# Kernel optimization log

Hardware: AMD Instinct MI355X
Metric: run time of the kernel (lower is better)

The kernel has to match this reference:

```python
import jax, jax.numpy as jnp
import numpy as np

B, T, D = 2, 2048, 2048
H = 16
DK = 64          # head_k_dim (key_dim = D*0.5 = 1024)
DV = 128         # head_v_dim (value_dim = D*1.0 = 2048)
R = 16           # gate_low_rank_dim
GLN = 16.0       # gate_logit_normalizer
C = 64           # chunk size
EPS = 1e-5


def setup_inputs() -> dict:
    key = jax.random.key(0)
    ks = jax.random.split(key, 12)
    s = 0.02
    return {
        "hidden_states": jax.random.normal(ks[0], (B, T, D), jnp.float32),
        "Wq": jax.random.normal(ks[1], (D, H * DK), jnp.float32) * s,
        "Wk": jax.random.normal(ks[2], (D, H * DK), jnp.float32) * s,
        "Wv": jax.random.normal(ks[3], (D, H * DV), jnp.float32) * s,
        "Wgk1": jax.random.normal(ks[4], (D, R), jnp.float32) * s,
        "Wgk2": jax.random.normal(ks[5], (R, H * DK), jnp.float32) * s,
        "bgk2": jnp.zeros((H * DK,), jnp.float32),
        "Wg1": jax.random.normal(ks[6], (D, R), jnp.float32) * s,
        "Wg2": jax.random.normal(ks[7], (R, H * DV), jnp.float32) * s,
        "bg2": jnp.zeros((H * DV,), jnp.float32),
        "Wo": jax.random.normal(ks[8], (H * DV, D), jnp.float32) * s,
        "gnorm_w": jnp.ones((DV,), jnp.float32),
    }


def _gla_chunk(q, k, v, gk):
    """Chunked gated linear attention.
    q,k,gk: [B,T,H,DK], v: [B,T,H,DV]. Recurrence:
    S_t = diag(exp(gk_t)) S_{t-1} + k_t v_t^T ; o_t = q_t @ S_t.
    """
    nC = T // C
    # [nC, B, H, C, d]
    def to_chunks(x):
        return x.reshape(B, nC, C, H, -1).transpose(1, 0, 3, 2, 4)
    qc, kc, vc, gkc = map(to_chunks, (q, k, v, gk))
    Gc = jnp.cumsum(gkc, axis=3)  # inclusive cumsum of log-decays within chunk
    tri = jnp.tril(jnp.ones((C, C), bool))

    def step(S, inp):
        q_c, k_c, v_c, G_c = inp  # [B,H,C,dk] / [B,H,C,dv]
        qg = q_c * jnp.exp(G_c)            # decays <= 0 within chunk -> safe
        kg = k_c * jnp.exp(-G_c)
        # inter-chunk: state contribution
        o = jnp.einsum('bhcd,bhde->bhce', qg, S)
        # intra-chunk causal attention with decay
        A = jnp.einsum('bhid,bhjd->bhij', qg, kg)
        A = jnp.where(tri, A, 0.0)
        o = o + jnp.einsum('bhij,bhje->bhie', A, v_c)
        # state update
        G_last = G_c[:, :, -1, :]                       # [B,H,dk]
        k_dec = k_c * jnp.exp(G_last[:, :, None, :] - G_c)
        S = S * jnp.exp(G_last)[:, :, :, None] + jnp.einsum('bhcd,bhce->bhde', k_dec, v_c)
        return S, o

    S0 = jnp.zeros((B, H, DK, DV), q.dtype)
    _, o = jax.lax.scan(step, S0, (qc, kc, vc, Gc))
    # [nC,B,H,C,dv] -> [B,T,H,dv]
    return o.transpose(1, 0, 3, 2, 4).reshape(B, T, H, DV)


def reference(hidden_states, Wq, Wk, Wv, Wgk1, Wgk2, bgk2, Wg1, Wg2, bg2, Wo, gnorm_w):
    hs = hidden_states
    q = jax.nn.silu(hs @ Wq).reshape(B, T, H, DK)
    k = jax.nn.silu(hs @ Wk).reshape(B, T, H, DK)
    v = jax.nn.silu(hs @ Wv).reshape(B, T, H, DV)
    gk = ((hs @ Wgk1) @ Wgk2 + bgk2).reshape(B, T, H, DK)
    gk = jax.nn.log_sigmoid(gk) / GLN
    q = q * (DK ** -0.5)  # fla default scale
    o = _gla_chunk(q, k, v, gk)  # [B,T,H,DV]
    # RMSNorm over head_v_dim
    o = o * jax.lax.rsqrt(jnp.mean(o * o, axis=-1, keepdims=True) + EPS) * gnorm_w
    g = ((hs @ Wg1) @ Wg2 + bg2).reshape(B, T, H, DV)
    o = o * jax.nn.sigmoid(g)
    return o.reshape(B, T, H * DV) @ Wo
```

## Files before the change

### kernel.cpp

```cpp
#include <hip/hip_runtime.h>
#include <cstdint>

#define Bq   2
#define Tq   2048
#define Dq   2048
#define Hq   16
#define DKq  64
#define DVq  128
#define Cq   64
#define NCq  32
#define Mq   4096
#define NBH  32

typedef _Float16 f16;
typedef f16 f16x4 __attribute__((ext_vector_type(4)));
typedef f16 f16x8 __attribute__((ext_vector_type(8)));
typedef float f32x4 __attribute__((ext_vector_type(4)));
typedef unsigned short u16;
typedef u16 u16x8 __attribute__((ext_vector_type(8)));

__device__ __forceinline__ void gl_lds16(const void* g, void* l) {
    __builtin_amdgcn_global_load_lds(
        (const __attribute__((address_space(1))) uint32_t*)g,
        (__attribute__((address_space(3))) uint32_t*)l, 16, 0, 0);
}

#define BARX()   asm volatile("s_barrier" ::: "memory")
#define LGKM0()  asm volatile("s_waitcnt lgkmcnt(0)" ::: "memory")
#define VMW8()   asm volatile("s_waitcnt vmcnt(8)" ::: "memory")
#define VMW6()   asm volatile("s_waitcnt vmcnt(6)" ::: "memory")

__global__ __launch_bounds__(256) void trans_all(const float* __restrict__ Wq,
                                                 const float* __restrict__ Wk,
                                                 const float* __restrict__ Wv,
                                                 const float* __restrict__ Wo,
                                                 f16* __restrict__ Qkv, f16* __restrict__ WoT) {
    __shared__ float sh[4096];
    int blk = blockIdx.x;
    int tid = threadIdx.x;
    const float* W; f16* Dh; int N, nt, kt; long rowoff;
    if (blk < 2048)      { W = Wq; N = 1024; int t = blk;        nt = t & 31; kt = t >> 5; Dh = Qkv; rowoff = 0; }
    else if (blk < 4096) { W = Wk; N = 1024; int t = blk - 2048; nt = t & 31; kt = t >> 5; Dh = Qkv; rowoff = 1024; }
    else if (blk < 8192) { W = Wv; N = 2048; int t = blk - 4096; nt = t & 63; kt = t >> 6; Dh = Qkv; rowoff = 2048; }
    else                 { W = Wo; N = 2048; int t = blk - 8192; nt = t & 63; kt = t >> 6; Dh = WoT; rowoff = 0; }
    int tx = tid & 31, ty = tid >> 5;
#pragma unroll
    for (int i = 0; i < 4; i++) {
        int k = kt * 32 + ty + i * 8;
        int n = nt * 32 + tx;
        sh[tx * 33 + ty + i * 8] = W[(long)k * N + n];
    }
    __syncthreads();
#pragma unroll
    for (int i = 0; i < 4; i++) {
        int n = nt * 32 + ty + i * 8;
        int k = kt * 32 + tx;
        Dh[(rowoff + n) * 2048L + k] = (f16)sh[(ty + i * 8) * 33 + tx];
    }
}

__global__ __launch_bounds__(256) void hs_conv(const float* __restrict__ in,
                                               f16* __restrict__ out) {
    long i = ((long)blockIdx.x * 256 + threadIdx.x) * 8;
    float4 a = *(const float4*)(in + i);
    float4 b = *(const float4*)(in + i + 4);
    f16x8 h;
    h[0] = (f16)a.x; h[1] = (f16)a.y; h[2] = (f16)a.z; h[3] = (f16)a.w;
    h[4] = (f16)b.x; h[5] = (f16)b.y; h[6] = (f16)b.z; h[7] = (f16)b.w;
    *(f16x8*)(out + i) = h;
}

__global__ __launch_bounds__(256) void lowrank_tg(const float* __restrict__ hs,
                                                  const float* __restrict__ Wgk1,
                                                  const float* __restrict__ Wg1,
                                                  float* __restrict__ t_gk,
                                                  float* __restrict__ t_g) {
    __shared__ float sW[512 * 32];
    int tid = threadIdx.x;
    int blk = blockIdx.x;
    int r = tid >> 4, seg = tid & 15;
    long row = (long)blk * 16 + r;
    float acc[32];
#pragma unroll
    for (int c = 0; c < 32; c++) acc[c] = 0.f;
    for (int kc = 0; kc < 2048; kc += 512) {
        __syncthreads();
#pragma unroll
        for (int i = 0; i < 16; i++) {
            int s = tid + i * 256;
            int k = s >> 3, q = s & 7;
            float4 w = (q < 4) ? *(const float4*)(Wgk1 + (long)(kc + k) * 16 + q * 4)
                               : *(const float4*)(Wg1  + (long)(kc + k) * 16 + (q - 4) * 4);
            int qs = q ^ ((k >> 5) & 7);
            *(float4*)&sW[k * 32 + qs * 4] = w;
        }
        __syncthreads();
        const float* hp = hs + row * 2048 + kc + seg * 32;
        int xr = seg & 7;
#pragma unroll
        for (int k4 = 0; k4 < 8; k4++) {
            float4 hv = *(const float4*)(hp + k4 * 4);
            float hvv[4] = {hv.x, hv.y, hv.z, hv.w};
#pragma unroll
            for (int u = 0; u < 4; u++) {
                int k = seg * 32 + k4 * 4 + u;
                const float* wr = &sW[k * 32];
#pragma unroll
                for (int q = 0; q < 8; q++) {
                    float4 wv = *(const float4*)(wr + ((q ^ xr) * 4));
                    acc[q * 4 + 0] += hvv[u] * wv.x;
                    acc[q * 4 + 1] += hvv[u] * wv.y;
                    acc[q * 4 + 2] += hvv[u] * wv.z;
                    acc[q * 4 + 3] += hvv[u] * wv.w;
                }
            }
        }
    }
#pragma unroll
    for (int c = 0; c < 32; c++) {
        acc[c] += __shfl_xor(acc[c], 1);
        acc[c] += __shfl_xor(acc[c], 2);
        acc[c] += __shfl_xor(acc[c], 4);
        acc[c] += __shfl_xor(acc[c], 8);
    }
    if (seg == 0) {
        float4 a;
        a.x = acc[0];  a.y = acc[1];  a.z = acc[2];  a.w = acc[3];  *(float4*)(t_gk + row * 16)     = a;
        a.x = acc[4];  a.y = acc[5];  a.z = acc[6];  a.w = acc[7];  *(float4*)(t_gk + row * 16 + 4) = a;
        a.x = acc[8];  a.y = acc[9];  a.z = acc[10]; a.w = acc[11]; *(float4*)(t_gk + row * 16 + 8) = a;
        a.x = acc[12]; a.y = acc[13]; a.z = acc[14]; a.w = acc[15]; *(float4*)(t_gk + row * 16 + 12)= a;
        a.x = acc[16]; a.y = acc[17]; a.z = acc[18]; a.w = acc[19]; *(float4*)(t_g + row * 16)      = a;
        a.x = acc[20]; a.y = acc[21]; a.z = acc[22]; a.w = acc[23]; *(float4*)(t_g + row * 16 + 4)  = a;
        a.x = acc[24]; a.y = acc[25]; a.z = acc[26]; a.w = acc[27]; *(float4*)(t_g + row * 16 + 8)  = a;
        a.x = acc[28]; a.y = acc[29]; a.z = acc[30]; a.w = acc[31]; *(float4*)(t_g + row * 16 + 12) = a;
    }
}

__global__ __launch_bounds__(512, 2) void gemm256q(const f16* __restrict__ A,
                                                   const f16* __restrict__ Bt,
                                                   f16* __restrict__ h0,
                                                   f16* __restrict__ h1,
                                                   f16* __restrict__ h2) {
    __shared__ __align__(16) f16 sA[2][16384];
    __shared__ __align__(16) f16 sB[2][16384];
    int tid = threadIdx.x;
    int wave = tid >> 6, lane = tid & 63;
    int quad = lane >> 4, l16 = lane & 15;
    int wm = wave >> 2, wn = wave & 3;

    int cpx = (int)gridDim.x >> 3;
    int wid = ((int)blockIdx.x & 7) * cpx + ((int)blockIdx.x >> 3);
    int bm = wid & 15, bn = wid >> 4;

    const f16* Ab = A  + (long)bm * 256 * 2048;
    const f16* Bb = Bt + (long)bn * 256 * 2048;

    int srow = tid >> 3;
    int gsrc = ((tid & 7) ^ (srow & 7)) * 8;
    const f16* Asrc = Ab + (long)srow * 2048 + gsrc;
    const f16* Bsrc = Bb + (long)srow * 2048 + gsrc;

#define STAGE(P, KT) do { \
    const f16* as_ = Asrc + (KT) * 64; \
    const f16* bs_ = Bsrc + (KT) * 64; \
    f16* la_ = &sA[P][tid * 8]; \
    f16* lb_ = &sB[P][tid * 8]; \
    _Pragma("unroll") \
    for (int q_ = 0; q_ < 4; q_++) gl_lds16(as_ + (long)q_ * 64 * 2048, la_ + q_ * 4096); \
    _Pragma("unroll") \
    for (int q_ = 0; q_ < 4; q_++) gl_lds16(bs_ + (long)q_ * 64 * 2048, lb_ + q_ * 4096); \
} while (0)

    int go0 = (quad ^ (l16 & 7)) * 8;
    int go1 = go0 ^ 32;
    const f16* aB0 = &sA[0][(wm * 128 + l16) * 64];
    const f16* aB1 = &sA[1][(wm * 128 + l16) * 64];
    const f16* bB0 = &sB[0][(wn * 64 + l16) * 64];
    const f16* bB1 = &sB[1][(wn * 64 + l16) * 64];

    f16x8 afr[4][2], bfr[2][2][2];
    f32x4 acc[8][4] = {};

#define LDA(PB, MH) do { \
    _Pragma("unroll") \
    for (int ii_ = 0; ii_ < 4; ii_++) { \
        afr[ii_][0] = *(const f16x8*)(PB + ((MH) * 4 + ii_) * 1024 + go0); \
        afr[ii_][1] = *(const f16x8*)(PB + ((MH) * 4 + ii_) * 1024 + go1); \
    } \
} while (0)

#define LDB(PB, NH) do { \
    _Pragma("unroll") \
    for (int jj_ = 0; jj_ < 2; jj_++) { \
        bfr[NH][jj_][0] = *(const f16x8*)(PB + ((NH) * 2 + jj_) * 1024 + go0); \
        bfr[NH][jj_][1] = *(const f16x8*)(PB + ((NH) * 2 + jj_) * 1024 + go1); \
    } \
} while (0)

#define QMFMA(MH, NH) do { \
    __builtin_amdgcn_s_setprio(1); \
    _Pragma("unroll") \
    for (int ii_ = 0; ii_ < 4; ii_++) \
    _Pragma("unroll") \
    for (int jj_ = 0; jj_ < 2; jj_++) { \
        acc[(MH)*4+ii_][(NH)*2+jj_] = __builtin_amdgcn_mfma_f32_16x16x32_f16(afr[ii_][0], bfr[NH][jj_][0], acc[(MH)*4+ii_][(NH)*2+jj_], 0, 0, 0); \
        acc[(MH)*4+ii_][(NH)*2+jj_] = __builtin_amdgcn_mfma_f32_16x16x32_f16(afr[ii_][1], bfr[NH][jj_][1], acc[(MH)*4+ii_][(NH)*2+jj_], 0, 0, 0); \
    } \
    __builtin_amdgcn_s_setprio(0); \
} while (0)

    STAGE(0, 0);
    STAGE(1, 1);
    VMW8();
    BARX();

#pragma unroll 1
    for (int it = 0; it < 16; it++) {
        int kt2 = 2 * it + 2; if (kt2 > 31) kt2 = 31;
        int kt3 = 2 * it + 3; if (kt3 > 31) kt3 = 31;
        LDA(aB0, 0); LDB(bB0, 0);
        BARX(); LGKM0(); QMFMA(0, 0); BARX();
        LDB(bB0, 1);
        BARX(); LGKM0(); QMFMA(0, 1); BARX();
        LDA(aB0, 1);
        BARX(); LGKM0(); QMFMA(1, 0); BARX();
        STAGE(0, kt2);
        VMW8();
        BARX(); QMFMA(1, 1); BARX();
        LDA(aB1, 0); LDB(bB1, 0);
        BARX(); LGKM0(); QMFMA(0, 0); BARX();
        LDB(bB1, 1);
        BARX(); LGKM0(); QMFMA(0, 1); BARX();
        LDA(aB1, 1);
        BARX(); LGKM0(); QMFMA(1, 0); BARX();
        STAGE(1, kt3);
        VMW8();
        BARX(); QMFMA(1, 1); BARX();
    }
    asm volatile("s_waitcnt vmcnt(0)" ::: "memory");

    long rb = (long)bm * 256 + wm * 128 + quad * 4;
    f16* dst; long cw, cb; float sc = 1.f;
    if (bn < 4)      { dst = h0; cw = 1024; cb = (long)bn * 256;       sc = 0.125f; }
    else if (bn < 8) { dst = h1; cw = 1024; cb = (long)(bn - 4) * 256; }
    else             { dst = h2; cw = 2048; cb = (long)(bn - 8) * 256; }
    long cbase = cb + wn * 64 + l16;
#pragma unroll
    for (int i = 0; i < 8; i++)
#pragma unroll
        for (int j = 0; j < 4; j++)
#pragma unroll
            for (int r = 0; r < 4; r++) {
                float x = acc[i][j][r];
                x = x / (1.f + __expf(-x)) * sc;
                dst[(rb + i * 16 + r) * cw + cbase + j * 16] = (f16)x;
            }
#undef STAGE
#undef LDA
#undef LDB
#undef QMFMA
}

__global__ __launch_bounds__(512, 2) void gemm128o(const f16* __restrict__ A,
                                                   const f16* __restrict__ Bt,
                                                   float* __restrict__ o0) {
    __shared__ __align__(16) f16 sAb[16384];
    __shared__ __align__(16) f16 sBb[32768];
    int tid = threadIdx.x;
    int wave = tid >> 6, lane = tid & 63;
    int quad = lane >> 4, l16 = lane & 15;
    int wm = wave >> 2, wn = wave & 3;

    int cpx = (int)gridDim.x >> 3;
    int wid = ((int)blockIdx.x & 7) * cpx + ((int)blockIdx.x >> 3);
    int bm = wid & 31, bn = wid >> 5;

    int srow = tid >> 3;
    int gsrc = ((tid & 7) ^ (srow & 7)) * 8;
    const f16* Asrc = A  + ((long)bm * 128 + srow) * 2048 + gsrc;
    const f16* Bsrc = Bt + ((long)bn * 256 + srow) * 2048 + gsrc;

#define STAGE(P, KT) do { \
    _Pragma("unroll") \
    for (int q_ = 0; q_ < 2; q_++) \
        gl_lds16(Asrc + (KT) * 64 + (long)q_ * 64 * 2048, sAb + (P) * 8192 + tid * 8 + q_ * 4096); \
    _Pragma("unroll") \
    for (int q_ = 0; q_ < 4; q_++) \
        gl_lds16(Bsrc + (KT) * 64 + (long)q_ * 64 * 2048, sBb + (P) * 16384 + tid * 8 + q_ * 4096); \
} while (0)

    int go0 = (quad ^ (l16 & 7)) * 8;
    int go1 = go0 ^ 32;
    const f16* pA0 = sAb + (wm * 64 + l16) * 64 + go0;
    const f16* pA1 = sAb + (wm * 64 + l16) * 64 + go1;
    const f16* pB0 = sBb + (wn * 64 + l16) * 64 + go0;
    const f16* pB1 = sBb + (wn * 64 + l16) * 64 + go1;

    f16x8 aX[4], bX[4], aY[4], bY[4];
    f32x4 acc[4][4] = {};

#define RDA(D, PTR, POFF) do { \
    D[0] = *(const f16x8*)((PTR) + (POFF)); \
    D[1] = *(const f16x8*)((PTR) + (POFF) + 1024); \
    D[2] = *(const f16x8*)((PTR) + (POFF) + 2048); \
    D[3] = *(const f16x8*)((PTR) + (POFF) + 3072); \
} while (0)

#define MM(AS, BS) do { \
    __builtin_amdgcn_s_setprio(1); \
    _Pragma("unroll") \
    for (int m_ = 0; m_ < 4; m_++) \
    _Pragma("unroll") \
    for (int n_ = 0; n_ < 4; n_++) \
        acc[m_][n_] = __builtin_amdgcn_mfma_f32_16x16x32_f16(AS[m_], BS[n_], acc[m_][n_], 0, 0, 0); \
    __builtin_amdgcn_s_setprio(0); \
} while (0)

    STAGE(0, 0);
    STAGE(1, 1);
    VMW6();
    BARX();
    RDA(aX, pA0, 0); RDA(bX, pB0, 0);

#pragma unroll 1
    for (int it = 0; it < 16; it++) {
        int c2 = 2 * it + 2; if (c2 > 31) c2 = 31;
        int c3 = 2 * it + 3; if (c3 > 31) c3 = 31;
        RDA(aY, pA1, 0); RDA(bY, pB1, 0);
        MM(aX, bX);
        LGKM0();
        BARX();
        STAGE(0, c2);
        VMW6();
        BARX();
        RDA(aX, pA0, 8192); RDA(bX, pB0, 16384);
        MM(aY, bY);
        RDA(aY, pA1, 8192); RDA(bY, pB1, 16384);
        MM(aX, bX);
        LGKM0();
        BARX();
        STAGE(1, c3);
        VMW6();
        BARX();
        RDA(aX, pA0, 0); RDA(bX, pB0, 0);
        MM(aY, bY);
    }
    asm volatile("s_waitcnt vmcnt(0)" ::: "memory");

    long rb = (long)bm * 128 + wm * 64 + quad * 4;
    long cbase = (long)bn * 256 + wn * 64 + l16;
#pragma unroll
    for (int m = 0; m < 4; m++)
#pragma unroll
        for (int n = 0; n < 4; n++)
#pragma unroll
            for (int r = 0; r < 4; r++)
                o0[(rb + m * 16 + r) * 2048 + cbase + n * 16] = acc[m][n][r];
#undef STAGE
#undef RDA
#undef MM
}

__global__ __launch_bounds__(256) void vtrans(const u16* __restrict__ v,
                                              u16* __restrict__ vT) {
    __shared__ uint32_t su[128 * 65];
    int tid = threadIdx.x;
    int t0 = (blockIdx.x >> 5) * 128;
    int e0 = (blockIdx.x & 31) * 64;
#pragma unroll
    for (int i = 0; i < 4; i++) {
        int tr = i * 32 + (tid >> 3);
        int ec = (tid & 7) * 8;
        u16x8 g = *(const u16x8*)(v + (long)(t0 + tr) * 2048 + e0 + ec);
#pragma unroll
        for (int j = 0; j < 8; j++) su[tr * 65 + ec + j] = g[j];
    }
    __syncthreads();
#pragma unroll
    for (int i = 0; i < 2; i++) {
        int er = i * 32 + (tid >> 3);
        int tch = (tid & 7) * 16;
        u16x8 o0, o1;
#pragma unroll
        for (int j = 0; j < 8; j++) {
            o0[j] = (u16)su[(tch + j) * 65 + er];
            o1[j] = (u16)su[(tch + 8 + j) * 65 + er];
        }
        u16* dst = vT + (long)(e0 + er) * 4096 + t0 + tch;
        *(u16x8*)dst = o0;
        *(u16x8*)(dst + 8) = o1;
    }
}

__global__ __launch_bounds__(256) void gk_cum(const float* __restrict__ t_gk,
                                              const float* __restrict__ Wgk2,
                                              const float* __restrict__ bgk2,
                                              float* __restrict__ G,
                                              float* __restrict__ dec) {
    __shared__ float sT[1024];
    __shared__ float sW[1024];
    __shared__ float sb[64];
    __shared__ float sG[64 * 64];
    int blk = blockIdx.x;
    int c = blk & 31, h = (blk >> 5) & 15, b = blk >> 9;
    int tid = threadIdx.x;
    long rowbase = (long)b * Tq + c * 64;
    {
        int idx = tid * 4;
        *(float4*)&sT[idx] = *(const float4*)(t_gk + rowbase * 16 + idx);
        int rr = idx >> 6, dd = idx & 63;
        *(float4*)&sW[idx] = *(const float4*)(Wgk2 + rr * 1024 + h * 64 + dd);
    }
    if (tid < 64) sb[tid] = bgk2[h * 64 + tid];
    __syncthreads();
    int tquad = tid >> 4, dgrp = tid & 15;
    float4 bg4 = *(float4*)&sb[dgrp * 4];
#pragma unroll
    for (int j = 0; j < 4; j++) {
        int t = tquad * 4 + j;
        float4 z = bg4;
#pragma unroll
        for (int rr = 0; rr < 16; rr++) {
            float tv = sT[t * 16 + rr];
            float4 wv = *(float4*)&sW[rr * 64 + dgrp * 4];
            z.x += tv * wv.x; z.y += tv * wv.y; z.z += tv * wv.z; z.w += tv * wv.w;
        }
        float4 o;
        o.x = (fminf(z.x, 0.f) - log1pf(__expf(-fabsf(z.x)))) * 0.0625f;
        o.y = (fminf(z.y, 0.f) - log1pf(__expf(-fabsf(z.y)))) * 0.0625f;
        o.z = (fminf(z.z, 0.f) - log1pf(__expf(-fabsf(z.z)))) * 0.0625f;
        o.w = (fminf(z.w, 0.f) - log1pf(__expf(-fabsf(z.w)))) * 0.0625f;
        *(float4*)&sG[t * 64 + dgrp * 4] = o;
    }
    __syncthreads();
    if (tid < 64) {
        float run = 0.f;
        for (int t = 0; t < 64; t++) { run += sG[t * 64 + tid]; sG[t * 64 + tid] = run; }
        dec[blk * 64 + tid] = __expf(run);
    }
    __syncthreads();
    float* Gb = G + (long)blk * 4096;
#pragma unroll
    for (int i = 0; i < 4; i++) {
        int f = tid + i * 256;
        *(float4*)(Gb + f * 4) = *(float4*)&sG[f * 4];
    }
}

#define ST 68
__global__ __launch_bounds__(256) void gla_pass1(const f16* __restrict__ kbuf,
                                                 const f16* __restrict__ vh,
                                                 const float* __restrict__ G,
                                                 float* __restrict__ U) {
    __shared__ float sG[64 * ST];
    __shared__ float sK[64 * ST];
    int blk = blockIdx.x;
    int c = blk & 31, h = (blk >> 5) & 15, b = blk >> 9;
    int tid = threadIdx.x;
    long rowbase = (long)b * Tq + c * 64;
    const float* Gb = G + (long)blk * 4096;
#pragma unroll
    for (int i = 0; i < 4; i++) {
        int f = tid + i * 256;
        float4 v = *(const float4*)(Gb + f * 4);
        int t = f >> 4, d0 = (f & 15) * 4;
        *(float4*)&sG[t * ST + d0] = v;
    }
    __syncthreads();
#pragma unroll
    for (int i = 0; i < 16; i++) {
        int idx = tid + i * 256;
        int t = idx >> 6, d = idx & 63;
        float gl = sG[63 * ST + d];
        sK[t * ST + d] = (float)kbuf[(rowbase + t) * 1024 + h * 64 + d] * __expf(gl - sG[t * ST + d]);
    }
    __syncthreads();
    int ty = tid >> 4, tx = tid & 15;
    float acc[4][8] = {};
    const f16* vb = vh + rowbase * 2048 + h * 128 + tx * 8;
    for (int t = 0; t < 64; t++) {
        float kd[4];
        *(float4*)&kd[0] = *(float4*)&sK[t * ST + ty * 4];
        f16x8 vv = *(const f16x8*)(vb + (long)t * 2048);
        float ve[8];
#pragma unroll
        for (int e = 0; e < 8; e++) ve[e] = (float)vv[e];
#pragma unroll
        for (int r = 0; r < 4; r++)
#pragma unroll
            for (int e = 0; e < 8; e++) acc[r][e] += kd[r] * ve[e];
    }
    float* Ub = U + (long)blk * 8192;
#pragma unroll
    for (int r = 0; r < 4; r++) {
        int d = ty * 4 + r;
#pragma unroll
        for (int e8 = 0; e8 < 8; e8++)
            Ub[(tx * 8 + e8) * 64 + d] = acc[r][e8];
    }
}

__global__ __launch_bounds__(256) void gla_pass2(const float* __restrict__ U,
                                                 const float* __restrict__ dec,
                                                 f16* __restrict__ ShT) {
    int bh = blockIdx.x >> 2;
    int tid = threadIdx.x;
    int e = (blockIdx.x & 3) * 32 + (tid >> 3);
    int d0 = (tid & 7) * 8;
    float4 Sa = {0.f, 0.f, 0.f, 0.f}, Sb = {0.f, 0.f, 0.f, 0.f};
    for (int c = 0; c < NCq; c++) {
        long base = ((long)(bh * 32 + c) * 128 + e) * 64 + d0;
        float4 u0 = *(const float4*)(U + base);
        float4 u1 = *(const float4*)(U + base + 4);
        const float* dp = dec + (bh * 32 + c) * 64 + d0;
        float4 dc0 = *(const float4*)dp;
        float4 dc1 = *(const float4*)(dp + 4);
        f16x8 sh;
        sh[0] = (f16)Sa.x; sh[1] = (f16)Sa.y; sh[2] = (f16)Sa.z; sh[3] = (f16)Sa.w;
        sh[4] = (f16)Sb.x; sh[5] = (f16)Sb.y; sh[6] = (f16)Sb.z; sh[7] = (f16)Sb.w;
        *(f16x8*)(ShT + base) = sh;
        Sa.x = Sa.x * dc0.x + u0.x; Sa.y = Sa.y * dc0.y + u0.y;
        Sa.z = Sa.z * dc0.z + u0.z; Sa.w = Sa.w * dc0.w + u0.w;
        Sb.x = Sb.x * dc1.x + u1.x; Sb.y = Sb.y * dc1.y + u1.y;
        Sb.z = Sb.z * dc1.z + u1.z; Sb.w = Sb.w * dc1.w + u1.w;
    }
}

#define GRD(row, kslot) (((row) << 6) + ((((kslot) ^ ((row) & 7))) << 3))
__global__ __launch_bounds__(256) void gla_pass3(const f16* __restrict__ qb,
                                                 const f16* __restrict__ kb,
                                                 const float* __restrict__ G,
                                                 const float* __restrict__ t_g,
                                                 const float* __restrict__ Wg2,
                                                 const float* __restrict__ bg2,
                                                 const float* __restrict__ gnw,
                                                 const f16* __restrict__ ShT,
                                                 const f16* __restrict__ vT,
                                                 f16* __restrict__ Oh) {
    __shared__ __align__(16) f16 sQg[4096];
    __shared__ __align__(16) f16 sKg[4096];
    __shared__ __align__(16) f16 sAh[4096];
    __shared__ __align__(16) f16 sST[8192];
    __shared__ __align__(16) f16 sVT[8192];
    __shared__ float sWg[16 * 128];
    __shared__ float sbg[128];
    int blk = blockIdx.x;
    int c = blk & 31, h = (blk >> 5) & 15, b = blk >> 9;
    int tid = threadIdx.x;
    long rowbase = (long)b * Tq + c * 64;

#pragma unroll
    for (int i = 0; i < 4; i++) {
        int s = tid + i * 256;
        int e = s >> 3, gp = s & 7;
        int gl = gp ^ (e & 7);
        gl_lds16(ShT + (long)blk * 8192 + e * 64 + gl * 8, sST + s * 8);
        gl_lds16(vT + (long)(h * 128 + e) * 4096 + rowbase + gl * 8, sVT + s * 8);
    }
#pragma unroll
    for (int i = 0; i < 2; i++) {
        int idx = tid * 4 + i * 1024;
        int rr = idx >> 7, ee = idx & 127;
        *(float4*)&sWg[idx] = *(const float4*)(Wg2 + (long)rr * 2048 + h * 128 + ee);
    }
    if (tid < 128) sbg[tid] = bg2[h * 128 + tid];
#pragma unroll
    for (int i = 0; i < 4; i++) {
        int f = tid + i * 256;
        int t = f >> 4, gi = f & 15;
        float4 G4 = *(const float4*)(G + (long)blk * 4096 + f * 4);
        long gb = (rowbase + t) * 1024 + h * 64 + gi * 4;
        f16x4 q4 = *(const f16x4*)(qb + gb);
        f16x4 k4 = *(const f16x4*)(kb + gb);
        f16x4 qh, kh;
        float ex;
        ex = __expf(G4.x); qh[0] = (f16)((float)q4[0] * ex); kh[0] = (f16)((float)k4[0] / ex);
        ex = __expf(G4.y); qh[1] = (f16)((float)q4[1] * ex); kh[1] = (f16)((float)k4[1] / ex);
        ex = __expf(G4.z); qh[2] = (f16)((float)q4[2] * ex); kh[2] = (f16)((float)k4[2] / ex);
        ex = __expf(G4.w); qh[3] = (f16)((float)q4[3] * ex); kh[3] = (f16)((float)k4[3] / ex);
        int w = (t << 6) + ((((gi >> 1) ^ (t & 7))) << 3) + ((gi & 1) << 2);
        *(f16x4*)(sQg + w) = qh;
        *(f16x4*)(sKg + w) = kh;
    }
    __syncthreads();

    int wv = tid >> 6, lane = tid & 63;
    int quad = lane >> 4, l16 = lane & 15;
    int trow = wv * 16 + l16;

    f16x8 afq[2];
    afq[0] = *(const f16x8*)(sQg + GRD(trow, quad));
    afq[1] = *(const f16x8*)(sQg + GRD(trow, 4 + quad));
#pragma unroll
    for (int j4 = 0; j4 < 4; j4++) {
        int tc = j4 * 16 + l16;
        f16x8 bk0 = *(const f16x8*)(sKg + GRD(tc, quad));
        f16x8 bk1 = *(const f16x8*)(sKg + GRD(tc, 4 + quad));
        f32x4 ca = {};
        ca = __builtin_amdgcn_mfma_f32_16x16x32_f16(afq[0], bk0, ca, 0, 0, 0);
        ca = __builtin_amdgcn_mfma_f32_16x16x32_f16(afq[1], bk1, ca, 0, 0, 0);
#pragma unroll
        for (int r = 0; r < 4; r++) {
            int tr = wv * 16 + quad * 4 + r;
            int tcw = j4 * 16 + l16;
            f16 av = (tcw <= tr) ? (f16)ca[r] : (f16)0.f;
            sAh[(tr << 6) + ((((tcw >> 3) ^ (tr & 7))) << 3) + (tcw & 7)] = av;
        }
    }

    f16x8 afa[2];
    afa[0] = *(const f16x8*)(sAh + GRD(trow, quad));
    afa[1] = *(const f16x8*)(sAh + GRD(trow, 4 + quad));
    f32x4 acc[8];
#pragma unroll
    for (int et = 0; et < 8; et++) {
        int e = et * 16 + l16;
        f16x8 bs0 = *(const f16x8*)(sST + GRD(e, quad));
        f16x8 bs1 = *(const f16x8*)(sST + GRD(e, 4 + quad));
        f16x8 bv0 = *(const f16x8*)(sVT + GRD(e, quad));
        f16x8 bv1 = *(const f16x8*)(sVT + GRD(e, 4 + quad));
        f32x4 cc = {};
        cc = __builtin_amdgcn_mfma_f32_16x16x32_f16(afq[0], bs0, cc, 0, 0, 0);
        cc = __builtin_amdgcn_mfma_f32_16x16x32_f16(afq[1], bs1, cc, 0, 0, 0);
        cc = __builtin_amdgcn_mfma_f32_16x16x32_f16(afa[0], bv0, cc, 0, 0, 0);
        cc = __builtin_amdgcn_mfma_f32_16x16x32_f16(afa[1], bv1, cc, 0, 0, 0);
        acc[et] = cc;
    }

    float gw[8], bgv[8];
#pragma unroll
    for (int et = 0; et < 8; et++) {
        gw[et]  = gnw[et * 16 + l16];
        bgv[et] = sbg[et * 16 + l16];
    }
#pragma unroll
    for (int half = 0; half < 2; half++) {
        float tg[2][16];
#pragma unroll
        for (int rh = 0; rh < 2; rh++) {
            int t = wv * 16 + quad * 4 + half * 2 + rh;
            const float* tgp = t_g + (rowbase + t) * 16;
#pragma unroll
            for (int q4 = 0; q4 < 4; q4++)
                *(float4*)&tg[rh][q4 * 4] = *(const float4*)(tgp + q4 * 4);
        }
        float g[2][8];
#pragma unroll
        for (int rh = 0; rh < 2; rh++)
#pragma unroll
            for (int et = 0; et < 8; et++) g[rh][et] = bgv[et];
#pragma unroll
        for (int rr = 0; rr < 16; rr++) {
#pragma unroll
            for (int et = 0; et < 8; et++) {
                float wv_ = sWg[rr * 128 + et * 16 + l16];
                g[0][et] += tg[0][rr] * wv_;
                g[1][et] += tg[1][rr] * wv_;
            }
        }
#pragma unroll
        for (int rh = 0; rh < 2; rh++) {
            int r = half * 2 + rh;
            int t = wv * 16 + quad * 4 + r;
            float ss = 0.f;
#pragma unroll
            for (int et = 0; et < 8; et++) ss += acc[et][r] * acc[et][r];
            ss += __shfl_xor(ss, 1);
            ss += __shfl_xor(ss, 2);
            ss += __shfl_xor(ss, 4);
            ss += __shfl_xor(ss, 8);
            float scale = rsqrtf(ss * (1.f / 128.f) + 1e-5f);
            long off = (rowbase + t) * 2048 + h * 128 + l16;
#pragma unroll
            for (int et = 0; et < 8; et++) {
                float y = acc[et][r] * scale * gw[et] / (1.f + __expf(-g[rh][et]));
                Oh[off + et * 16] = (f16)y;
            }
        }
    }
}

extern "C" void kernel_launch(void* const* d_in, const int* in_sizes, int n_in,
                              void* d_out, int out_size, void* d_ws, size_t ws_size,
                              hipStream_t stream) {
    const float* hs   = (const float*)d_in[0];
    const float* Wq   = (const float*)d_in[1];
    const float* Wk   = (const float*)d_in[2];
    const float* Wv   = (const float*)d_in[3];
    const float* Wgk1 = (const float*)d_in[4];
    const float* Wgk2 = (const float*)d_in[5];
    const float* bgk2 = (const float*)d_in[6];
    const float* Wg1  = (const float*)d_in[7];
    const float* Wg2  = (const float*)d_in[8];
    const float* bg2  = (const float*)d_in[9];
    const float* Wo   = (const float*)d_in[10];
    const float* gnw  = (const float*)d_in[11];

    char* w = (char*)d_ws;
    auto alloc = [&](size_t bytes) {
        char* p = w; w += (bytes + 255) & ~size_t(255); return (void*)p;
    };
    f16*   Xh     = (f16*)  alloc((size_t)Mq * Dq * 2);
    f16*   WqkvT  = (f16*)  alloc((size_t)4224 * 2048 * 2);
    f16*   WoT    = (f16*)  alloc((size_t)2048 * 2048 * 2);
    f16*   qb     = (f16*)  alloc((size_t)Mq * 1024 * 2);
    f16*   kb     = (f16*)  alloc((size_t)Mq * 1024 * 2);
    f16*   vhb    = (f16*)  alloc((size_t)Mq * 2048 * 2);
    f16*   vTb    = (f16*)  alloc((size_t)Mq * 2048 * 2);
    float* t_gk   = (float*)alloc((size_t)Mq * 16 * 4);
    float* t_g    = (float*)alloc((size_t)Mq * 16 * 4);
    float* Ut     = (float*)alloc((size_t)NBH * NCq * 8192 * 4);
    f16*   ShT    = (f16*)  alloc((size_t)NBH * NCq * 8192 * 2);
    float* dec    = (float*)alloc((size_t)NBH * NCq * 64 * 4);
    float* Gbuf   = (float*)alloc((size_t)NBH * NCq * 4096 * 4);

    trans_all<<<12288, 256, 0, stream>>>(Wq, Wk, Wv, Wo, WqkvT, WoT);
    hs_conv<<<Mq * Dq / 2048, 256, 0, stream>>>(hs, Xh);
    lowrank_tg<<<256, 256, 0, stream>>>(hs, Wgk1, Wg1, t_gk, t_g);

    gemm256q<<<256, 512, 0, stream>>>(Xh, WqkvT, qb, kb, vhb);
    vtrans<<<1024, 256, 0, stream>>>((const u16*)vhb, (u16*)vTb);

    gk_cum<<<NBH * NCq, 256, 0, stream>>>(t_gk, Wgk2, bgk2, Gbuf, dec);
    gla_pass1<<<NBH * NCq, 256, 0, stream>>>(kb, vhb, Gbuf, Ut);
    gla_pass2<<<NBH * 4, 256, 0, stream>>>(Ut, dec, ShT);
    gla_pass3<<<NBH * NCq, 256, 0, stream>>>(qb, kb, Gbuf, t_g, Wg2, bg2, gnw, ShT, vTb, Xh);

    gemm128o<<<256, 512, 0, stream>>>(Xh, WoT, (float*)d_out);
}
```

Measured before the change: 396.6 us.

## Merge prep kernels into combined launches, split gemm staging, widen pass2 grid

Merges the weight-transpose, hidden-state conversion and low-rank gate kernels into one launch. The v-transpose and gk cumsum kernels become a second merged launch, cutting launch count and letting independent work share the GPU. The QKV GEMM's global-to-LDS staging is split into separate A and B halves issued at different points in the pipeline, so memory traffic is spread across the MFMA phases. The sequential state-scan kernel now uses twice as many blocks with 4-wide vectors, giving more parallelism on the serial chunk loop. The merged kernels reserve the larger shared-memory footprint for every block, which may lower occupancy for the lighter branches.

After: 419.2 us. +5.7%, slower.

```diff
diff --git a/kernel.cpp b/kernel.cpp
--- a/kernel.cpp
+++ b/kernel.cpp
@@ -30,109 +30,108 @@
 #define VMW8()   asm volatile("s_waitcnt vmcnt(8)" ::: "memory")
 #define VMW6()   asm volatile("s_waitcnt vmcnt(6)" ::: "memory")
 
-__global__ __launch_bounds__(256) void trans_all(const float* __restrict__ Wq,
-                                                 const float* __restrict__ Wk,
-                                                 const float* __restrict__ Wv,
-                                                 const float* __restrict__ Wo,
-                                                 f16* __restrict__ Qkv, f16* __restrict__ WoT) {
-    __shared__ float sh[4096];
+__global__ __launch_bounds__(256) void prep1(const float* __restrict__ Wq,
+                                             const float* __restrict__ Wk,
+                                             const float* __restrict__ Wv,
+                                             const float* __restrict__ Wo,
+                                             const float* __restrict__ hs,
+                                             const float* __restrict__ Wgk1,
+                                             const float* __restrict__ Wg1,
+                                             f16* __restrict__ Qkv, f16* __restrict__ WoT,
+                                             f16* __restrict__ Xh,
+                                             float* __restrict__ t_gk,
+                                             float* __restrict__ t_g) {
+    __shared__ __align__(16) char smem_raw[65536];
     int blk = blockIdx.x;
     int tid = threadIdx.x;
-    const float* W; f16* Dh; int N, nt, kt; long rowoff;
-    if (blk < 2048)      { W = Wq; N = 1024; int t = blk;        nt = t & 31; kt = t >> 5; Dh = Qkv; rowoff = 0; }
-    else if (blk < 4096) { W = Wk; N = 1024; int t = blk - 2048; nt = t & 31; kt = t >> 5; Dh = Qkv; rowoff = 1024; }
-    else if (blk < 8192) { W = Wv; N = 2048; int t = blk - 4096; nt = t & 63; kt = t >> 6; Dh = Qkv; rowoff = 2048; }
-    else                 { W = Wo; N = 2048; int t = blk - 8192; nt = t & 63; kt = t >> 6; Dh = WoT; rowoff = 0; }
-    int tx = tid & 31, ty = tid >> 5;
-#pragma unroll
-    for (int i = 0; i < 4; i++) {
-        int k = kt * 32 + ty + i * 8;
-        int n = nt * 32 + tx;
-        sh[tx * 33 + ty + i * 8] = W[(long)k * N + n];
-    }
-    __syncthreads();
-#pragma unroll
-    for (int i = 0; i < 4; i++) {
-        int n = nt * 32 + ty + i * 8;
-        int k = kt * 32 + tx;
-        Dh[(rowoff + n) * 2048L + k] = (f16)sh[(ty + i * 8) * 33 + tx];
-    }
-}
-
-__global__ __launch_bounds__(256) void hs_conv(const float* __restrict__ in,
-                                               f16* __restrict__ out) {
-    long i = ((long)blockIdx.x * 256 + threadIdx.x) * 8;
-    float4 a = *(const float4*)(in + i);
-    float4 b = *(const float4*)(in + i + 4);
-    f16x8 h;
-    h[0] = (f16)a.x; h[1] = (f16)a.y; h[2] = (f16)a.z; h[3] = (f16)a.w;
-    h[4] = (f16)b.x; h[5] = (f16)b.y; h[6] = (f16)b.z; h[7] = (f16)b.w;
-    *(f16x8*)(out + i) = h;
-}
-
-__global__ __launch_bounds__(256) void lowrank_tg(const float* __restrict__ hs,
-                                                  const float* __restrict__ Wgk1,
-                                                  const float* __restrict__ Wg1,
-                                                  float* __restrict__ t_gk,
-                                                  float* __restrict__ t_g) {
-    __shared__ float sW[512 * 32];
-    int tid = threadIdx.x;
-    int blk = blockIdx.x;
-    int r = tid >> 4, seg = tid & 15;
-    long row = (long)blk * 16 + r;
-    float acc[32];
-#pragma unroll
-    for (int c = 0; c < 32; c++) acc[c] = 0.f;
-    for (int kc = 0; kc < 2048; kc += 512) {
+    if (blk < 12288) {
+        float* sh = (float*)smem_raw;
+        const float* W; f16* Dh; int N, nt, kt; long rowoff;
+        if (blk < 2048)      { W = Wq; N = 1024; int t = blk;        nt = t & 31; kt = t >> 5; Dh = Qkv; rowoff = 0; }
+        else if (blk < 4096) { W = Wk; N = 1024; int t = blk - 2048; nt = t & 31; kt = t >> 5; Dh = Qkv; rowoff = 1024; }
+        else if (blk < 8192) { W = Wv; N = 2048; int t = blk - 4096; nt = t & 63; kt = t >> 6; Dh = Qkv; rowoff = 2048; }
+        else                 { W = Wo; N = 2048; int t = blk - 8192; nt = t & 63; kt = t >> 6; Dh = WoT; rowoff = 0; }
+        int tx = tid & 31, ty = tid >> 5;
+#pragma unroll
+        for (int i = 0; i < 4; i++) {
+            int k = kt * 32 + ty + i * 8;
+            int n = nt * 32 + tx;
+            sh[tx * 33 + ty + i * 8] = W[(long)k * N + n];
+        }
         __syncthreads();
 #pragma unroll
-        for (int i = 0; i < 16; i++) {
-            int s = tid + i * 256;
-            int k = s >> 3, q = s & 7;
-            float4 w = (q < 4) ? *(const float4*)(Wgk1 + (long)(kc + k) * 16 + q * 4)
-                               : *(const float4*)(Wg1  + (long)(kc + k) * 16 + (q - 4) * 4);
-            int qs = q ^ ((k >> 5) & 7);
-            *(float4*)&sW[k * 32 + qs * 4] = w;
-        }
-        __syncthreads();
-        const float* hp = hs + row * 2048 + kc + seg * 32;
-        int xr = seg & 7;
-#pragma unroll
-        for (int k4 = 0; k4 < 8; k4++) {
-            float4 hv = *(const float4*)(hp + k4 * 4);
-            float hvv[4] = {hv.x, hv.y, hv.z, hv.w};
-#pragma unroll
-            for (int u = 0; u < 4; u++) {
-                int k = seg * 32 + k4 * 4 + u;
-                const float* wr = &sW[k * 32];
-#pragma unroll
-                for (int q = 0; q < 8; q++) {
-                    float4 wv = *(const float4*)(wr + ((q ^ xr) * 4));
-                    acc[q * 4 + 0] += hvv[u] * wv.x;
-                    acc[q * 4 + 1] += hvv[u] * wv.y;
-                    acc[q * 4 + 2] += hvv[u] * wv.z;
-                    acc[q * 4 + 3] += hvv[u] * wv.w;
+        for (int i = 0; i < 4; i++) {
+            int n = nt * 32 + ty + i * 8;
+            int k = kt * 32 + tx;
+            Dh[(rowoff + n) * 2048L + k] = (f16)sh[(ty + i * 8) * 33 + tx];
+        }
+    } else if (blk < 16384) {
+        long i = ((long)(blk - 12288) * 256 + tid) * 8;
+        float4 a = *(const float4*)(hs + i);
+        float4 b = *(const float4*)(hs + i + 4);
+        f16x8 h;
+        h[0] = (f16)a.x; h[1] = (f16)a.y; h[2] = (f16)a.z; h[3] = (f16)a.w;
+        h[4] = (f16)b.x; h[5] = (f16)b.y; h[6] = (f16)b.z; h[7] = (f16)b.w;
+        *(f16x8*)(Xh + i) = h;
+    } else {
+        float* sW = (float*)smem_raw;
+        int bq = blk - 16384;
+        int r = tid >> 4, seg = tid & 15;
+        long row = (long)bq * 16 + r;
+        float acc[32];
+#pragma unroll
+        for (int c = 0; c < 32; c++) acc[c] = 0.f;
+        for (int kc = 0; kc < 2048; kc += 512) {
+            __syncthreads();
+#pragma unroll
+            for (int i = 0; i < 16; i++) {
+                int s = tid + i * 256;
+                int k = s >> 3, q = s & 7;
+                float4 w = (q < 4) ? *(const float4*)(Wgk1 + (long)(kc + k) * 16 + q * 4)
+                                   : *(const float4*)(Wg1  + (long)(kc + k) * 16 + (q - 4) * 4);
+                int qs = q ^ ((k >> 5) & 7);
+                *(float4*)&sW[k * 32 + qs * 4] = w;
+            }
+            __syncthreads();
+            const float* hp = hs + row * 2048 + kc + seg * 32;
+            int xr = seg & 7;
+#pragma unroll
+            for (int k4 = 0; k4 < 8; k4++) {
+                float4 hv = *(const float4*)(hp + k4 * 4);
+                float hvv[4] = {hv.x, hv.y, hv.z, hv.w};
+#pragma unroll
+                for (int u = 0; u < 4; u++) {
+                    int k = seg * 32 + k4 * 4 + u;
+                    const float* wr = &sW[k * 32];
+#pragma unroll
+                    for (int q = 0; q < 8; q++) {
+                        float4 wv = *(const float4*)(wr + ((q ^ xr) * 4));
+                        acc[q * 4 + 0] += hvv[u] * wv.x;
+                        acc[q * 4 + 1] += hvv[u] * wv.y;
+                        acc[q * 4 + 2] += hvv[u] * wv.z;
+                        acc[q * 4 + 3] += hvv[u] * wv.w;
+                    }
                 }
             }
         }
-    }
-#pragma unroll
-    for (int c = 0; c < 32; c++) {
-        acc[c] += __shfl_xor(acc[c], 1);
-        acc[c] += __shfl_xor(acc[c], 2);
-        acc[c] += __shfl_xor(acc[c], 4);
-        acc[c] += __shfl_xor(acc[c], 8);
-    }
-    if (seg == 0) {
-        float4 a;
-        a.x = acc[0];  a.y = acc[1];  a.z = acc[2];  a.w = acc[3];  *(float4*)(t_gk + row * 16)     = a;
-        a.x = acc[4];  a.y = acc[5];  a.z = acc[6];  a.w = acc[7];  *(float4*)(t_gk + row * 16 + 4) = a;
-        a.x = acc[8];  a.y = acc[9];  a.z = acc[10]; a.w = acc[11]; *(float4*)(t_gk + row * 16 + 8) = a;
-        a.x = acc[12]; a.y = acc[13]; a.z = acc[14]; a.w = acc[15]; *(float4*)(t_gk + row * 16 + 12)= a;
-        a.x = acc[16]; a.y = acc[17]; a.z = acc[18]; a.w = acc[19]; *(float4*)(t_g + row * 16)      = a;
-        a.x = acc[20]; a.y = acc[21]; a.z = acc[22]; a.w = acc[23]; *(float4*)(t_g + row * 16 + 4)  = a;
-        a.x = acc[24]; a.y = acc[25]; a.z = acc[26]; a.w = acc[27]; *(float4*)(t_g + row * 16 + 8)  = a;
-        a.x = acc[28]; a.y = acc[29]; a.z = acc[30]; a.w = acc[31]; *(float4*)(t_g + row * 16 + 12) = a;
+#pragma unroll
+        for (int c = 0; c < 32; c++) {
+            acc[c] += __shfl_xor(acc[c], 1);
+            acc[c] += __shfl_xor(acc[c], 2);
+            acc[c] += __shfl_xor(acc[c], 4);
+            acc[c] += __shfl_xor(acc[c], 8);
+        }
+        if (seg == 0) {
+            float4 a;
+            a.x = acc[0];  a.y = acc[1];  a.z = acc[2];  a.w = acc[3];  *(float4*)(t_gk + row * 16)     = a;
+            a.x = acc[4];  a.y = acc[5];  a.z = acc[6];  a.w = acc[7];  *(float4*)(t_gk + row * 16 + 4) = a;
+            a.x = acc[8];  a.y = acc[9];  a.z = acc[10]; a.w = acc[11]; *(float4*)(t_gk + row * 16 + 8) = a;
+            a.x = acc[12]; a.y = acc[13]; a.z = acc[14]; a.w = acc[15]; *(float4*)(t_gk + row * 16 + 12)= a;
+            a.x = acc[16]; a.y = acc[17]; a.z = acc[18]; a.w = acc[19]; *(float4*)(t_g + row * 16)      = a;
+            a.x = acc[20]; a.y = acc[21]; a.z = acc[22]; a.w = acc[23]; *(float4*)(t_g + row * 16 + 4)  = a;
+            a.x = acc[24]; a.y = acc[25]; a.z = acc[26]; a.w = acc[27]; *(float4*)(t_g + row * 16 + 8)  = a;
+            a.x = acc[28]; a.y = acc[29]; a.z = acc[30]; a.w = acc[31]; *(float4*)(t_g + row * 16 + 12) = a;
+        }
     }
 }
 
@@ -160,15 +159,15 @@
     const f16* Asrc = Ab + (long)srow * 2048 + gsrc;
     const f16* Bsrc = Bb + (long)srow * 2048 + gsrc;
 
-#define STAGE(P, KT) do { \
-    const f16* as_ = Asrc + (KT) * 64; \
-    const f16* bs_ = Bsrc + (KT) * 64; \
-    f16* la_ = &sA[P][tid * 8]; \
-    f16* lb_ = &sB[P][tid * 8]; \
-    _Pragma("unroll") \
-    for (int q_ = 0; q_ < 4; q_++) gl_lds16(as_ + (long)q_ * 64 * 2048, la_ + q_ * 4096); \
-    _Pragma("unroll") \
-    for (int q_ = 0; q_ < 4; q_++) gl_lds16(bs_ + (long)q_ * 64 * 2048, lb_ + q_ * 4096); \
+#define STG_A(P, KT) do { \
+    _Pragma("unroll") \
+    for (int q_ = 0; q_ < 4; q_++) \
+        gl_lds16(Asrc + (KT) * 64 + (long)q_ * 64 * 2048, &sA[P][tid * 8] + q_ * 4096); \
+} while (0)
+#define STG_B(P, KT) do { \
+    _Pragma("unroll") \
+    for (int q_ = 0; q_ < 4; q_++) \
+        gl_lds16(Bsrc + (KT) * 64 + (long)q_ * 64 * 2048, &sB[P][tid * 8] + q_ * 4096); \
 } while (0)
 
     int go0 = (quad ^ (l16 & 7)) * 8;
@@ -209,8 +208,8 @@
     __builtin_amdgcn_s_setprio(0); \
 } while (0)
 
-    STAGE(0, 0);
-    STAGE(1, 1);
+    STG_A(0, 0); STG_B(0, 0);
+    STG_A(1, 1); STG_B(1, 1);
     VMW8();
     BARX();
 
@@ -222,18 +221,18 @@
         BARX(); LGKM0(); QMFMA(0, 0); BARX();
         LDB(bB0, 1);
         BARX(); LGKM0(); QMFMA(0, 1); BARX();
-        LDA(aB0, 1);
+        LDA(aB0, 1); STG_B(0, kt2);
         BARX(); LGKM0(); QMFMA(1, 0); BARX();
-        STAGE(0, kt2);
+        STG_A(0, kt2);
         VMW8();
         BARX(); QMFMA(1, 1); BARX();
         LDA(aB1, 0); LDB(bB1, 0);
         BARX(); LGKM0(); QMFMA(0, 0); BARX();
         LDB(bB1, 1);
         BARX(); LGKM0(); QMFMA(0, 1); BARX();
-        LDA(aB1, 1);
+        LDA(aB1, 1); STG_B(1, kt3);
         BARX(); LGKM0(); QMFMA(1, 0); BARX();
-        STAGE(1, kt3);
+        STG_A(1, kt3);
         VMW8();
         BARX(); QMFMA(1, 1); BARX();
     }
@@ -255,7 +254,8 @@
                 x = x / (1.f + __expf(-x)) * sc;
                 dst[(rb + i * 16 + r) * cw + cbase + j * 16] = (f16)x;
             }
-#undef STAGE
+#undef STG_A
+#undef STG_B
 #undef LDA
 #undef LDB
 #undef QMFMA
@@ -361,89 +361,91 @@
 #undef MM
 }
 
-__global__ __launch_bounds__(256) void vtrans(const u16* __restrict__ v,
-                                              u16* __restrict__ vT) {
-    __shared__ uint32_t su[128 * 65];
+__global__ __launch_bounds__(256) void prep2(const u16* __restrict__ v,
+                                             u16* __restrict__ vT,
+                                             const float* __restrict__ t_gk,
+                                             const float* __restrict__ Wgk2,
+                                             const float* __restrict__ bgk2,
+                                             float* __restrict__ G,
+                                             float* __restrict__ dec) {
+    __shared__ __align__(16) char smem_raw[33280];
+    int blk = blockIdx.x;
     int tid = threadIdx.x;
-    int t0 = (blockIdx.x >> 5) * 128;
-    int e0 = (blockIdx.x & 31) * 64;
-#pragma unroll
-    for (int i = 0; i < 4; i++) {
-        int tr = i * 32 + (tid >> 3);
-        int ec = (tid & 7) * 8;
-        u16x8 g = *(const u16x8*)(v + (long)(t0 + tr) * 2048 + e0 + ec);
-#pragma unroll
-        for (int j = 0; j < 8; j++) su[tr * 65 + ec + j] = g[j];
-    }
-    __syncthreads();
-#pragma unroll
-    for (int i = 0; i < 2; i++) {
-        int er = i * 32 + (tid >> 3);
-        int tch = (tid & 7) * 16;
-        u16x8 o0, o1;
-#pragma unroll
-        for (int j = 0; j < 8; j++) {
-            o0[j] = (u16)su[(tch + j) * 65 + er];
-            o1[j] = (u16)su[(tch + 8 + j) * 65 + er];
-        }
-        u16* dst = vT + (long)(e0 + er) * 4096 + t0 + tch;
-        *(u16x8*)dst = o0;
-        *(u16x8*)(dst + 8) = o1;
-    }
-}
-
-__global__ __launch_bounds__(256) void gk_cum(const float* __restrict__ t_gk,
-                                              const float* __restrict__ Wgk2,
-                                              const float* __restrict__ bgk2,
-                                              float* __restrict__ G,
-                                              float* __restrict__ dec) {
-    __shared__ float sT[1024];
-    __shared__ float sW[1024];
-    __shared__ float sb[64];
-    __shared__ float sG[64 * 64];
-    int blk = blockIdx.x;
-    int c = blk & 31, h = (blk >> 5) & 15, b = blk >> 9;
-    int tid = threadIdx.x;
-    long rowbase = (long)b * Tq + c * 64;
-    {
-        int idx = tid * 4;
-        *(float4*)&sT[idx] = *(const float4*)(t_gk + rowbase * 16 + idx);
-        int rr = idx >> 6, dd = idx & 63;
-        *(float4*)&sW[idx] = *(const float4*)(Wgk2 + rr * 1024 + h * 64 + dd);
-    }
-    if (tid < 64) sb[tid] = bgk2[h * 64 + tid];
-    __syncthreads();
-    int tquad = tid >> 4, dgrp = tid & 15;
-    float4 bg4 = *(float4*)&sb[dgrp * 4];
-#pragma unroll
-    for (int j = 0; j < 4; j++) {
-        int t = tquad * 4 + j;
-        float4 z = bg4;
-#pragma unroll
-        for (int rr = 0; rr < 16; rr++) {
-            float tv = sT[t * 16 + rr];
-            float4 wv = *(float4*)&sW[rr * 64 + dgrp * 4];
-            z.x += tv * wv.x; z.y += tv * wv.y; z.z += tv * wv.z; z.w += tv * wv.w;
-        }
-        float4 o;
-        o.x = (fminf(z.x, 0.f) - log1pf(__expf(-fabsf(z.x)))) * 0.0625f;
-        o.y = (fminf(z.y, 0.f) - log1pf(__expf(-fabsf(z.y)))) * 0.0625f;
-        o.z = (fminf(z.z, 0.f) - log1pf(__expf(-fabsf(z.z)))) * 0.0625f;
-        o.w = (fminf(z.w, 0.f) - log1pf(__expf(-fabsf(z.w)))) * 0.0625f;
-        *(float4*)&sG[t * 64 + dgrp * 4] = o;
-    }
-    __syncthreads();
-    if (tid < 64) {
-        float run = 0.f;
-        for (int t = 0; t < 64; t++) { run += sG[t * 64 + tid]; sG[t * 64 + tid] = run; }
-        dec[blk * 64 + tid] = __expf(run);
-    }
-    __syncthreads();
-    float* Gb = G + (long)blk * 4096;
-#pragma unroll
-    for (int i = 0; i < 4; i++) {
-        int f = tid + i * 256;
-        *(float4*)(Gb + f * 4) = *(float4*)&sG[f * 4];
+    if (blk < 1024) {
+        uint32_t* su = (uint32_t*)smem_raw;
+        int t0 = (blk >> 5) * 128;
+        int e0 = (blk & 31) * 64;
+#pragma unroll
+        for (int i = 0; i < 4; i++) {
+            int tr = i * 32 + (tid >> 3);
+            int ec = (tid & 7) * 8;
+            u16x8 g = *(const u16x8*)(v + (long)(t0 + tr) * 2048 + e0 + ec);
+#pragma unroll
+            for (int j = 0; j < 8; j++) su[tr * 65 + ec + j] = g[j];
+        }
+        __syncthreads();
+#pragma unroll
+        for (int i = 0; i < 2; i++) {
+            int er = i * 32 + (tid >> 3);
+            int tch = (tid & 7) * 16;
+            u16x8 o0, o1;
+#pragma unroll
+            for (int j = 0; j < 8; j++) {
+                o0[j] = (u16)su[(tch + j) * 65 + er];
+                o1[j] = (u16)su[(tch + 8 + j) * 65 + er];
+            }
+            u16* dst = vT + (long)(e0 + er) * 4096 + t0 + tch;
+            *(u16x8*)dst = o0;
+            *(u16x8*)(dst + 8) = o1;
+        }
+    } else {
+        float* sT = (float*)smem_raw;
+        float* sW = sT + 1024;
+        float* sb = sW + 1024;
+        float* sG = sb + 64;
+        int bq = blk - 1024;
+        int c = bq & 31, h = (bq >> 5) & 15, b = bq >> 9;
+        long rowbase = (long)b * Tq + c * 64;
+        {
+            int idx = tid * 4;
+            *(float4*)&sT[idx] = *(const float4*)(t_gk + rowbase * 16 + idx);
+            int rr = idx >> 6, dd = idx & 63;
+            *(float4*)&sW[idx] = *(const float4*)(Wgk2 + rr * 1024 + h * 64 + dd);
+        }
+        if (tid < 64) sb[tid] = bgk2[h * 64 + tid];
+        __syncthreads();
+        int tquad = tid >> 4, dgrp = tid & 15;
+        float4 bg4 = *(float4*)&sb[dgrp * 4];
+#pragma unroll
+        for (int j = 0; j < 4; j++) {
+            int t = tquad * 4 + j;
+            float4 z = bg4;
+#pragma unroll
+            for (int rr = 0; rr < 16; rr++) {
+                float tv = sT[t * 16 + rr];
+                float4 wv = *(float4*)&sW[rr * 64 + dgrp * 4];
+                z.x += tv * wv.x; z.y += tv * wv.y; z.z += tv * wv.z; z.w += tv * wv.w;
+            }
+            float4 o;
+            o.x = (fminf(z.x, 0.f) - log1pf(__expf(-fabsf(z.x)))) * 0.0625f;
+            o.y = (fminf(z.y, 0.f) - log1pf(__expf(-fabsf(z.y)))) * 0.0625f;
+            o.z = (fminf(z.z, 0.f) - log1pf(__expf(-fabsf(z.z)))) * 0.0625f;
+            o.w = (fminf(z.w, 0.f) - log1pf(__expf(-fabsf(z.w)))) * 0.0625f;
+            *(float4*)&sG[t * 64 + dgrp * 4] = o;
+        }
+        __syncthreads();
+        if (tid < 64) {
+            float run = 0.f;
+            for (int t = 0; t < 64; t++) { run += sG[t * 64 + tid]; sG[t * 64 + tid] = run; }
+            dec[bq * 64 + tid] = __expf(run);
+        }
+        __syncthreads();
+        float* Gb = G + (long)bq * 4096;
+#pragma unroll
+        for (int i = 0; i < 4; i++) {
+            int f = tid + i * 256;
+            *(float4*)(Gb + f * 4) = *(float4*)&sG[f * 4];
+        }
     }
 }
 
@@ -503,26 +505,20 @@
 __global__ __launch_bounds__(256) void gla_pass2(const float* __restrict__ U,
                                                  const float* __restrict__ dec,
                                                  f16* __restrict__ ShT) {
-    int bh = blockIdx.x >> 2;
+    int bh = blockIdx.x >> 3;
     int tid = threadIdx.x;
-    int e = (blockIdx.x & 3) * 32 + (tid >> 3);
-    int d0 = (tid & 7) * 8;
-    float4 Sa = {0.f, 0.f, 0.f, 0.f}, Sb = {0.f, 0.f, 0.f, 0.f};
+    int e = (blockIdx.x & 7) * 16 + (tid >> 4);
+    int d0 = (tid & 15) * 4;
+    float4 Sa = {0.f, 0.f, 0.f, 0.f};
     for (int c = 0; c < NCq; c++) {
         long base = ((long)(bh * 32 + c) * 128 + e) * 64 + d0;
         float4 u0 = *(const float4*)(U + base);
-        float4 u1 = *(const float4*)(U + base + 4);
-        const float* dp = dec + (bh * 32 + c) * 64 + d0;
-        float4 dc0 = *(const float4*)dp;
-        float4 dc1 = *(const float4*)(dp + 4);
-        f16x8 sh;
+        float4 dc0 = *(const float4*)(dec + (bh * 32 + c) * 64 + d0);
+        f16x4 sh;
         sh[0] = (f16)Sa.x; sh[1] = (f16)Sa.y; sh[2] = (f16)Sa.z; sh[3] = (f16)Sa.w;
-        sh[4] = (f16)Sb.x; sh[5] = (f16)Sb.y; sh[6] = (f16)Sb.z; sh[7] = (f16)Sb.w;
-        *(f16x8*)(ShT + base) = sh;
+        *(f16x4*)(ShT + base) = sh;
         Sa.x = Sa.x * dc0.x + u0.x; Sa.y = Sa.y * dc0.y + u0.y;
         Sa.z = Sa.z * dc0.z + u0.z; Sa.w = Sa.w * dc0.w + u0.w;
-        Sb.x = Sb.x * dc1.x + u1.x; Sb.y = Sb.y * dc1.y + u1.y;
-        Sb.z = Sb.z * dc1.z + u1.z; Sb.w = Sb.w * dc1.w + u1.w;
     }
 }
 
@@ -714,16 +710,16 @@
     float* dec    = (float*)alloc((size_t)NBH * NCq * 64 * 4);
     float* Gbuf   = (float*)alloc((size_t)NBH * NCq * 4096 * 4);
 
-    trans_all<<<12288, 256, 0, stream>>>(Wq, Wk, Wv, Wo, WqkvT, WoT);
-    hs_conv<<<Mq * Dq / 2048, 256, 0, stream>>>(hs, Xh);
-    lowrank_tg<<<256, 256, 0, stream>>>(hs, Wgk1, Wg1, t_gk, t_g);
+    prep1<<<16640, 256, 0, stream>>>(Wq, Wk, Wv, Wo, hs, Wgk1, Wg1,
+                                     WqkvT, WoT, Xh, t_gk, t_g);
 
     gemm256q<<<256, 512, 0, stream>>>(Xh, WqkvT, qb, kb, vhb);
-    vtrans<<<1024, 256, 0, stream>>>((const u16*)vhb, (u16*)vTb);
-
-    gk_cum<<<NBH * NCq, 256, 0, stream>>>(t_gk, Wgk2, bgk2, Gbuf, dec);
+
+    prep2<<<2048, 256, 0, stream>>>((const u16*)vhb, (u16*)vTb,
+                                    t_gk, Wgk2, bgk2, Gbuf, dec);
+
     gla_pass1<<<NBH * NCq, 256, 0, stream>>>(kb, vhb, Gbuf, Ut);
-    gla_pass2<<<NBH * 4, 256, 0, stream>>>(Ut, dec, ShT);
+    gla_pass2<<<NBH * 8, 256, 0, stream>>>(Ut, dec, ShT);
     gla_pass3<<<NBH * NCq, 256, 0, stream>>>(qb, kb, Gbuf, t_g, Wg2, bg2, gnw, ShT, vTb, Xh);
 
     gemm128o<<<256, 512, 0, stream>>>(Xh, WoT, (float*)d_out);
```
